# Optimization experiments

Hardware: AMD Instinct MI355X
Metric: run time of the kernel (lower is better)

## Reference

```python
import jax, jax.numpy as jnp
import numpy as np

D_MODEL = 512; N_HEADS = 8; D_HIDDEN = 512
STACK_DEPTH = 48; STACK_WIDTH = 128; D_FF = 2048; D_SS = 128
SEQ = 512; BATCH = 16
EP = 1e-4; MAX_ITER = 100


def nonsat(x):
    # fixed-point iteration y_ = (2y^3/3 + x)/(y^2+1); torch detaches y each step,
    # so grads flow only through x in the final step. Loop runs on stopped values.
    xs = jax.lax.stop_gradient(x)
    step = lambda y: (2.0 * y ** 3 / 3.0 + xs) / (y * y + 1.0)
    def cond(s):
        y, y_, i = s
        return jnp.logical_and(jnp.mean(jnp.abs(y_ - y)) > EP, i <= MAX_ITER)
    def body(s):
        y, y_, i = s
        return (y_, step(y_), i + 1)
    y_last, _, _ = jax.lax.while_loop(cond, body, (xs, step(xs), jnp.int32(0)))
    return (2.0 * y_last ** 3 / 3.0 + x) / (y_last * y_last + 1.0)


def layer_norm(x, g, b, eps=1e-5):
    m = jnp.mean(x, axis=-1, keepdims=True)
    v = jnp.mean((x - m) ** 2, axis=-1, keepdims=True)
    return (x - m) / jnp.sqrt(v + eps) * g + b


def mha(x, k_mask, wi, bi, wo, bo):
    # x: (S,B,E), torch nn.MultiheadAttention with combined in_proj, causal mask
    S, B, E = x.shape
    H = N_HEADS; hd = E // H
    qkv = x @ wi.T + bi
    q, k, v = jnp.split(qkv, 3, axis=-1)
    to_heads = lambda t: t.reshape(S, B, H, hd).transpose(1, 2, 0, 3)  # (B,H,S,hd)
    q = to_heads(q) * (hd ** -0.5)
    k = to_heads(k); v = to_heads(v)
    scores = jnp.einsum('bhqd,bhkd->bhqk', q, k)
    causal = jnp.triu(jnp.full((S, S), -jnp.inf, dtype=x.dtype), 1)
    scores = scores + causal
    scores = jnp.where(k_mask[:, None, None, :], -jnp.inf, scores)
    a = jax.nn.softmax(scores, axis=-1)
    o = jnp.einsum('bhqk,bhkd->bhqd', a, v).transpose(2, 0, 1, 3).reshape(S, B, E)
    return o @ wo.T + bo


def setup_inputs() -> dict:
    key = jax.random.key(0)
    ks = iter(jax.random.split(key, 32))
    E = D_MODEL
    def w(shape, fan_in):
        return (jax.random.normal(next(ks), shape, jnp.float32) / np.sqrt(fan_in)).astype(jnp.float32)
    inp = {
        'x_in': jax.random.normal(next(ks), (SEQ, BATCH, E), jnp.float32),
        'hidden_prev': jax.random.normal(next(ks), (BATCH, SEQ, D_HIDDEN), jnp.float32),
        'stack_prev': jax.random.normal(next(ks), (BATCH, SEQ, STACK_DEPTH, STACK_WIDTH), jnp.float32),
        'k_mask': jnp.zeros((BATCH, SEQ), dtype=bool),
        'in_proj_w': w((3 * E, E), E), 'in_proj_b': jnp.zeros((3 * E,), jnp.float32),
        'out_proj_w': w((E, E), E), 'out_proj_b': jnp.zeros((E,), jnp.float32),
        'ln1_g': jnp.ones((E,), jnp.float32), 'ln1_b': jnp.zeros((E,), jnp.float32),
        'ln2_g': jnp.ones((E,), jnp.float32), 'ln2_b': jnp.zeros((E,), jnp.float32),
        'ff_w1': w((D_FF, E), E), 'ff_b1': jnp.zeros((D_FF,), jnp.float32),
        'ff_w2': w((E, D_FF), D_FF), 'ff_b2': jnp.zeros((E,), jnp.float32),
        'W_w': w((D_HIDDEN, E), E), 'W_b': jnp.zeros((D_HIDDEN,), jnp.float32),
        'R_w': w((D_HIDDEN, D_HIDDEN), D_HIDDEN), 'R_b': jnp.zeros((D_HIDDEN,), jnp.float32),
        'P_w': w((D_HIDDEN, STACK_WIDTH), STACK_WIDTH), 'P_b': jnp.zeros((D_HIDDEN,), jnp.float32),
        'V_w': w((D_SS, E + D_HIDDEN), E + D_HIDDEN),
        'U_w': w((E, D_SS), D_SS),
        'A_w': w((3, D_HIDDEN), D_HIDDEN), 'A_b': jnp.zeros((3,), jnp.float32),
        'D_w': w((STACK_WIDTH, D_HIDDEN), D_HIDDEN), 'D_b': jnp.zeros((STACK_WIDTH,), jnp.float32),
    }
    return inp


def reference(x_in, hidden_prev, stack_prev, k_mask,
              in_proj_w, in_proj_b, out_proj_w, out_proj_b,
              ln1_g, ln1_b, ln2_g, ln2_b,
              ff_w1, ff_b1, ff_w2, ff_b2,
              W_w, W_b, R_w, R_b, P_w, P_b,
              V_w, U_w, A_w, A_b, D_w, D_b):
    # sublayer 1: pre-norm residual multihead self-attention
    x = x_in + mha(layer_norm(x_in, ln1_g, ln1_b), k_mask,
                   in_proj_w, in_proj_b, out_proj_w, out_proj_b)
    # stack-augmented memory update
    stack_x = stack_prev[:, :, 0, :]                       # (B,S,W) stack top
    xb = x.transpose(1, 0, 2)                              # (B,S,E)
    hidden = xb @ W_w.T + W_b + hidden_prev @ R_w.T + R_b + stack_x @ P_w.T + P_b
    hidden = nonsat(hidden)                                # (B,S,Dh)
    vx = jnp.concatenate([x, hidden.transpose(1, 0, 2)], axis=-1)  # (S,B,E+Dh)
    y = jax.nn.softmax(vx @ V_w.T, axis=-1) @ U_w.T        # (S,B,E)
    x = 0.5 * (x + y)
    stack_inp = nonsat(hidden @ D_w.T + D_b)[:, :, None, :]        # (B,S,1,W)
    controls = jax.nn.softmax(hidden @ A_w.T + A_b, axis=-1)       # (B,S,3)
    a_push = controls[:, :, 0, None, None]
    a_pop = controls[:, :, 1, None, None]
    a_noop = controls[:, :, 2, None, None]
    zeros_bot = jnp.zeros_like(stack_prev[:, :, :1])
    stack_down = jnp.concatenate([stack_prev[:, :, 1:], zeros_bot], axis=2)
    stack_up = jnp.concatenate([stack_inp, stack_prev[:, :, :-1]], axis=2)
    stack = a_noop * stack_prev + a_push * stack_up + a_pop * stack_down
    # sublayer 2: pre-norm residual position-wise FFN
    h = layer_norm(x, ln2_g, ln2_b)
    x = x + (jax.nn.relu(h @ ff_w1.T + ff_b1) @ ff_w2.T + ff_b2)
    return (x, hidden, stack)
```

## Files before the change

kernel.cpp:

```cpp
#include <hip/hip_runtime.h>
#include <stdint.h>

typedef unsigned short u16;
typedef short short8 __attribute__((ext_vector_type(8)));
typedef float f32x4 __attribute__((ext_vector_type(4)));

__device__ __forceinline__ u16 f2b(float f) {
    uint32_t x = __float_as_uint(f);
    uint32_t r = x + 0x7fffu + ((x >> 16) & 1u);
    return (u16)(r >> 16);
}

__device__ __forceinline__ float nonsat_f(float x) {
    float y = x;
#pragma unroll
    for (int t = 0; t < 14; ++t) {
        const float y2 = y * y;
        y = (0.66666667f * y2 * y + x) / (y2 + 1.f);
    }
    return y;
}

__device__ __forceinline__ void gl2lds16(const u16* g, u16* l) {
    __builtin_amdgcn_global_load_lds(
        (const __attribute__((address_space(1))) unsigned int*)g,
        (__attribute__((address_space(3))) unsigned int*)l, 16, 0, 0);
}

template <int MT, int MODE, bool RELU>
__global__ __launch_bounds__(256) void gemm_k(
    const u16* __restrict__ A, int lda,
    const u16* __restrict__ B, int ldb,
    const float* __restrict__ bias,
    int M, int N, int K,
    u16* __restrict__ out_b, float* __restrict__ out_f,
    const float* __restrict__ res_f, u16* __restrict__ out_b2)
{
    constexpr int MI = (MT >= 64) ? MT / 64 : 1;
    constexpr int WI = (MT >= 64) ? MT / 32 : 1;
    constexpr int ATILE = MT * 32;
    constexpr size_t STAGE_B = (size_t)(2 * ATILE + 8192) * 2;
    constexpr size_t EPIL_B = (MODE == 0 && MT == 128) ? (size_t)128 * 132 * 2
                             : (MODE == 8 ? (size_t)MT * 130 * 4 : 0);
    constexpr size_t SMEM_B = STAGE_B > EPIL_B ? STAGE_B : EPIL_B;

    const int tn = blockIdx.x, tm = blockIdx.y;
    const int tid = threadIdx.x;
    const int wave = tid >> 6, lane = tid & 63;
    const int quad = lane >> 4, mm = lane & 15;
    const int wr = (wave >> 1) * (MT / 2), wc = (wave & 1) * 64;

    __shared__ __align__(16) char SMEM[SMEM_B];
    u16* As = (u16*)SMEM;
    u16* Bs = (u16*)SMEM + 2 * ATILE;

    const f32x4 vzero = {0.f, 0.f, 0.f, 0.f};
    f32x4 acc[WI][4];
#pragma unroll
    for (int i = 0; i < WI; i++)
#pragma unroll
        for (int j = 0; j < 4; j++) acc[i][j] = vzero;

    const int lr = tid >> 2;
    const int lc = (tid & 3) * 8;
    const u16* ag[MI];
#pragma unroll
    for (int h = 0; h < MI; h++)
        ag[h] = A + (size_t)(tm * MT + (MT == 32 ? (lr & 31) : lr) + h * 64) * lda + lc;
    const u16* bg0 = B + (size_t)(tn * 128 + lr) * ldb + lc;
    const u16* bg1 = B + (size_t)(tn * 128 + lr + 64) * ldb + lc;

    auto STAGE = [&](int s, int kt) {
        if constexpr (MT == 32) {
            if (tid < 128) gl2lds16(ag[0] + kt, As + s * ATILE + wave * 512);
        } else {
#pragma unroll
            for (int h = 0; h < MI; h++)
                gl2lds16(ag[h] + kt, As + s * ATILE + h * 2048 + wave * 512);
        }
        gl2lds16(bg0 + kt, Bs + s * 4096 + wave * 512);
        gl2lds16(bg1 + kt, Bs + s * 4096 + 2048 + wave * 512);
    };

    const int nt = K >> 5;
    STAGE(0, 0);
    asm volatile("s_waitcnt vmcnt(0)" ::: "memory");
    __syncthreads();
    int cur = 0;

    for (int t = 0; t < nt; ++t) {
        if (t + 1 < nt) STAGE(cur ^ 1, (t + 1) * 32);
        const u16* as = As + cur * ATILE;
        const u16* bs = Bs + cur * 4096;
        short8 af[WI], bfr[4];
#pragma unroll
        for (int i = 0; i < WI; i++) af[i] = *(const short8*)(as + (wr + i * 16 + mm) * 32 + quad * 8);
#pragma unroll
        for (int j = 0; j < 4; j++) bfr[j] = *(const short8*)(bs + (wc + j * 16 + mm) * 32 + quad * 8);
#pragma unroll
        for (int i = 0; i < WI; i++)
#pragma unroll
            for (int j = 0; j < 4; j++)
                acc[i][j] = __builtin_amdgcn_mfma_f32_16x16x32_bf16(af[i], bfr[j], acc[i][j], 0, 0, 0);
        if (t + 1 < nt) {
            asm volatile("s_waitcnt vmcnt(0)" ::: "memory");
            __syncthreads();
            cur ^= 1;
        }
    }

    if constexpr (MODE == 0 && MT == 128) {
        __syncthreads();
        u16* Ct = (u16*)SMEM;
#pragma unroll
        for (int j = 0; j < 4; j++) {
            const int colg = tn * 128 + wc + j * 16 + mm;
            const float bv = bias ? bias[colg] : 0.f;
#pragma unroll
            for (int i = 0; i < WI; i++)
#pragma unroll
                for (int r = 0; r < 4; r++) {
                    float v = acc[i][j][r] + bv;
                    if (RELU) v = fmaxf(v, 0.f);
                    Ct[(wr + i * 16 + quad * 4 + r) * 132 + wc + j * 16 + mm] = f2b(v);
                }
        }
        __syncthreads();
        const int row = tid >> 1, half = tid & 1;
        const u16* src = Ct + row * 132 + half * 64;
        u16* dst = out_b + (size_t)(tm * 128 + row) * N + tn * 128 + half * 64;
#pragma unroll
        for (int c = 0; c < 8; c++)
            *(int4*)(dst + c * 8) = *(const int4*)(src + c * 8);
        return;
    }

    if constexpr (MODE == 8) {
        __syncthreads();
        float* Sm = (float*)SMEM;
#pragma unroll
        for (int j = 0; j < 4; j++)
#pragma unroll
            for (int i = 0; i < WI; i++)
#pragma unroll
                for (int r = 0; r < 4; r++)
                    Sm[(wr + i * 16 + quad * 4 + r) * 130 + wc + j * 16 + mm] = acc[i][j][r];
        __syncthreads();
#pragma unroll
        for (int rr = 0; rr < MT / 4; ++rr) {
            const int row_l = wave * (MT / 4) + rr;
            const float a = Sm[row_l * 130 + lane];
            const float b = Sm[row_l * 130 + 64 + lane];
            float mx = fmaxf(a, b);
#pragma unroll
            for (int off = 1; off < 64; off <<= 1) mx = fmaxf(mx, __shfl_xor(mx, off));
            const float ea = __expf(a - mx), eb = __expf(b - mx);
            float s = ea + eb;
#pragma unroll
            for (int off = 1; off < 64; off <<= 1) s += __shfl_xor(s, off);
            const float inv = 1.f / s;
            const size_t rowg = (size_t)tm * MT + row_l;
            out_b[rowg * 128 + lane] = f2b(ea * inv);
            out_b[rowg * 128 + 64 + lane] = f2b(eb * inv);
        }
        return;
    }

    float dotp[3][WI * 4];
    if constexpr (MODE == 6) {
#pragma unroll
        for (int w = 0; w < 3; w++)
#pragma unroll
            for (int q = 0; q < WI * 4; q++) dotp[w][q] = 0.f;
    }

#pragma unroll
    for (int j = 0; j < 4; j++) {
        const int colg = tn * 128 + wc + j * 16 + mm;
        const float bv = bias ? bias[colg] : 0.f;
        float aw0, aw1, aw2;
        if constexpr (MODE == 6) {
            aw0 = res_f[colg];
            aw1 = res_f[512 + colg];
            aw2 = res_f[1024 + colg];
        }
#pragma unroll
        for (int i = 0; i < WI; i++) {
#pragma unroll
            for (int r = 0; r < 4; r++) {
                const int rowg = tm * MT + wr + i * 16 + quad * 4 + r;
                float v = acc[i][j][r] + bv;
                const size_t off = (size_t)rowg * N + colg;
                if constexpr (MODE == 0) {
                    if (RELU) v = fmaxf(v, 0.f);
                    out_b[off] = f2b(v);
                } else if constexpr (MODE == 3) {
                    v += res_f[off];
                    out_f[off] = v;
                    const u16 hb = f2b(v);
                    out_b[(size_t)rowg * 1024 + colg] = hb;
                    out_b2[((size_t)(rowg & 15) * 512 + (rowg >> 4)) * 1152 + colg] = hb;
                } else if constexpr (MODE == 4) {
                    v = 0.5f * (v + res_f[off]);
                    out_f[off] = v;
                } else if constexpr (MODE == 5) {
                    v += res_f[off];
                    out_f[off] = v;
                } else if constexpr (MODE == 6) {
                    v = nonsat_f(v);
                    out_f[off] = v;
                    out_b[((size_t)(rowg & 511) * 16 + (rowg >> 9)) * 1024 + 512 + colg] = f2b(v);
                    dotp[0][i * 4 + r] += v * aw0;
                    dotp[1][i * 4 + r] += v * aw1;
                    dotp[2][i * 4 + r] += v * aw2;
                } else {
                    v = nonsat_f(v);
                    out_f[off] = v;
                }
            }
        }
    }

    if constexpr (MODE == 6) {
        float* lg = (float*)out_b2;
#pragma unroll
        for (int w = 0; w < 3; w++)
#pragma unroll
            for (int i = 0; i < WI; i++)
#pragma unroll
                for (int r = 0; r < 4; r++) {
                    float v = dotp[w][i * 4 + r];
                    v += __shfl_xor(v, 1);
                    v += __shfl_xor(v, 2);
                    v += __shfl_xor(v, 4);
                    v += __shfl_xor(v, 8);
                    if (mm == 0) {
                        const int rowg = tm * MT + wr + i * 16 + quad * 4 + r;
                        atomicAdd(&lg[(size_t)rowg * 3 + w], v);
                    }
                }
    }
}

struct CvtArgs {
    const float* s[12];
    unsigned cum[13];
};

static constexpr unsigned C_INPJ = 0;
static constexpr unsigned C_OUTP = 786432;
static constexpr unsigned C_FF1W = 1048576;
static constexpr unsigned C_FF2W = 2097152;
static constexpr unsigned C_WRP  = 3145728;
static constexpr unsigned C_VW   = 3735552;
static constexpr unsigned C_UW   = 3866624;
static constexpr unsigned C_DW   = 3932160;
static constexpr unsigned C_WTOT = 3997696;

__global__ __launch_bounds__(256) void cvt_k(CvtArgs a, u16* __restrict__ wa, u16* __restrict__ ha,
                                             const float* __restrict__ Wb, const float* __restrict__ Rb,
                                             const float* __restrict__ Pb, float* __restrict__ bsum,
                                             float* __restrict__ logz)
{
    if (blockIdx.x == gridDim.x - 1) {
        if (threadIdx.x < 128) {
            const int c = threadIdx.x * 4;
#pragma unroll
            for (int k = 0; k < 4; k++) bsum[c + k] = Wb[c + k] + Rb[c + k] + Pb[c + k];
        }
        return;
    }
    if (blockIdx.x == gridDim.x - 2) {
        float4 z = make_float4(0.f, 0.f, 0.f, 0.f);
        float4* p = (float4*)logz;
        for (int i = threadIdx.x; i < 6144; i += 256) p[i] = z;
        return;
    }
    const unsigned t = (blockIdx.x * 256u + threadIdx.x) * 8u;
    if (t >= a.cum[12]) return;
    int g = 0;
#pragma unroll
    for (int i = 1; i < 12; i++)
        if (t >= a.cum[i]) g = i;
    const unsigned e = t - a.cum[g];
    const float* src;
    u16* dst;
    if (g == 10) {
        src = a.s[10] + e;
        dst = ha + (size_t)(e >> 9) * 1152 + 512 + (e & 511);
    } else if (g == 11) {
        src = a.s[11] + (size_t)(e >> 7) * 6144 + (e & 127);
        dst = ha + (size_t)(e >> 7) * 1152 + 1024 + (e & 127);
    } else if (g == 4) {
        src = a.s[4] + e;
        dst = wa + C_WRP + (size_t)(e >> 9) * 1152 + (e & 511);
    } else if (g == 5) {
        src = a.s[5] + e;
        dst = wa + C_WRP + (size_t)(e >> 9) * 1152 + 512 + (e & 511);
    } else if (g == 6) {
        src = a.s[6] + e;
        dst = wa + C_WRP + (size_t)(e >> 7) * 1152 + 1024 + (e & 127);
    } else {
        src = a.s[g] + e;
        dst = wa + t;
    }
    float4 u0 = *(const float4*)src;
    float4 u1 = *(const float4*)(src + 4);
    __align__(16) u16 o[8] = {f2b(u0.x), f2b(u0.y), f2b(u0.z), f2b(u0.w),
                              f2b(u1.x), f2b(u1.y), f2b(u1.z), f2b(u1.w)};
    *(int4*)dst = *(const int4*)o;
}

__global__ __launch_bounds__(64) void attn_k(const u16* __restrict__ QKV, u16* __restrict__ O)
{
    const int qt = blockIdx.x;
    const int bh = blockIdx.y;
    const int b = bh >> 3, h = bh & 7;
    const int lane = threadIdx.x;
    const int quad = lane >> 4, mm = lane & 15;
    const int cbase = h * 64;
    const float NEGINF = -3.0e38f;

    __shared__ __align__(16) u16 Pl[64 * 72];
    __shared__ __align__(16) u16 Vl[64 * 72];

    short8 qf[4][2];
#pragma unroll
    for (int rt = 0; rt < 4; ++rt) {
        const int s = qt * 64 + rt * 16 + mm;
        const u16* p = QKV + ((size_t)s * 16 + b) * 1536 + cbase + quad * 8;
        qf[rt][0] = *(const short8*)(p);
        qf[rt][1] = *(const short8*)(p + 32);
    }

    const f32x4 vzero = {0.f, 0.f, 0.f, 0.f};
    f32x4 of[4][4];
#pragma unroll
    for (int i = 0; i < 4; i++)
#pragma unroll
        for (int j = 0; j < 4; j++) of[i][j] = vzero;
    float mrow[4][4], lrow[4][4];
#pragma unroll
    for (int i = 0; i < 4; i++)
#pragma unroll
        for (int r = 0; r < 4; r++) { mrow[i][r] = NEGINF; lrow[i][r] = 0.f; }

    for (int kt = 0; kt <= qt; ++kt) {
        short8 kf[4][2];
#pragma unroll
        for (int nt = 0; nt < 4; ++nt) {
            const int kk = kt * 64 + nt * 16 + mm;
            const u16* p = QKV + ((size_t)kk * 16 + b) * 1536 + 512 + cbase + quad * 8;
            kf[nt][0] = *(const short8*)(p);
            kf[nt][1] = *(const short8*)(p + 32);
        }
        f32x4 sf[4][4];
#pragma unroll
        for (int i = 0; i < 4; i++)
#pragma unroll
            for (int j = 0; j < 4; j++) sf[i][j] = vzero;
#pragma unroll
        for (int i = 0; i < 4; i++)
#pragma unroll
            for (int j = 0; j < 4; j++) {
                sf[i][j] = __builtin_amdgcn_mfma_f32_16x16x32_bf16(qf[i][0], kf[j][0], sf[i][j], 0, 0, 0);
                sf[i][j] = __builtin_amdgcn_mfma_f32_16x16x32_bf16(qf[i][1], kf[j][1], sf[i][j], 0, 0, 0);
            }
        {
            const int kk = lane >> 3, c8 = (lane & 7) * 8;
#pragma unroll
            for (int it = 0; it < 8; ++it) {
                const int key = kt * 64 + it * 8 + kk;
                int4 v = *(const int4*)(QKV + ((size_t)key * 16 + b) * 1536 + 1024 + cbase + c8);
                *(int4*)(Vl + (it * 8 + kk) * 72 + c8) = v;
            }
        }
        const bool diag = (kt == qt);
#pragma unroll
        for (int i = 0; i < 4; i++)
#pragma unroll
            for (int j = 0; j < 4; j++)
#pragma unroll
                for (int r = 0; r < 4; r++) {
                    float v = sf[i][j][r] * 0.125f;
                    if (diag) {
                        const int q = i * 16 + quad * 4 + r;
                        const int k = j * 16 + mm;
                        if (k > q) v = NEGINF;
                    }
                    sf[i][j][r] = v;
                }
#pragma unroll
        for (int i = 0; i < 4; i++) {
#pragma unroll
            for (int r = 0; r < 4; r++) {
                float mx = fmaxf(fmaxf(sf[i][0][r], sf[i][1][r]), fmaxf(sf[i][2][r], sf[i][3][r]));
                mx = fmaxf(mx, __shfl_xor(mx, 1));
                mx = fmaxf(mx, __shfl_xor(mx, 2));
                mx = fmaxf(mx, __shfl_xor(mx, 4));
                mx = fmaxf(mx, __shfl_xor(mx, 8));
                const float mnew = fmaxf(mrow[i][r], mx);
                const float alpha = __expf(mrow[i][r] - mnew);
                mrow[i][r] = mnew;
                float psum = 0.f;
#pragma unroll
                for (int j = 0; j < 4; j++) {
                    float p = __expf(sf[i][j][r] - mnew);
                    sf[i][j][r] = p;
                    psum += p;
                }
                psum += __shfl_xor(psum, 1);
                psum += __shfl_xor(psum, 2);
                psum += __shfl_xor(psum, 4);
                psum += __shfl_xor(psum, 8);
                lrow[i][r] = lrow[i][r] * alpha + psum;
#pragma unroll
                for (int j = 0; j < 4; j++) of[i][j][r] *= alpha;
            }
        }
#pragma unroll
        for (int i = 0; i < 4; i++)
#pragma unroll
            for (int j = 0; j < 4; j++)
#pragma unroll
                for (int r = 0; r < 4; r++)
                    Pl[(i * 16 + quad * 4 + r) * 72 + j * 16 + mm] = f2b(sf[i][j][r]);
        __syncthreads();
        short8 pa[4][2];
#pragma unroll
        for (int i = 0; i < 4; i++) {
            pa[i][0] = *(const short8*)(Pl + (i * 16 + mm) * 72 + quad * 8);
            pa[i][1] = *(const short8*)(Pl + (i * 16 + mm) * 72 + 32 + quad * 8);
        }
#pragma unroll
        for (int j = 0; j < 4; j++) {
#pragma unroll
            for (int kc = 0; kc < 2; ++kc) {
                short8 vb;
#pragma unroll
                for (int e = 0; e < 8; e++)
                    vb[e] = (short)Vl[(kc * 32 + quad * 8 + e) * 72 + j * 16 + mm];
#pragma unroll
                for (int i = 0; i < 4; i++)
                    of[i][j] = __builtin_amdgcn_mfma_f32_16x16x32_bf16(pa[i][kc], vb, of[i][j], 0, 0, 0);
            }
        }
        __syncthreads();
    }
#pragma unroll
    for (int i = 0; i < 4; i++)
#pragma unroll
        for (int r = 0; r < 4; r++) {
            const int s = qt * 64 + i * 16 + quad * 4 + r;
            const float inv = 1.f / lrow[i][r];
#pragma unroll
            for (int j = 0; j < 4; j++)
                O[((size_t)s * 16 + b) * 512 + cbase + j * 16 + mm] = f2b(of[i][j][r] * inv);
        }
}

__global__ __launch_bounds__(256) void ln_k(const float* __restrict__ x,
                                            const float* __restrict__ g,
                                            const float* __restrict__ be,
                                            u16* __restrict__ out)
{
    const int row = blockIdx.x * 4 + (threadIdx.x >> 6);
    const int lane = threadIdx.x & 63;
    const float* p = x + (size_t)row * 512 + lane * 8;
    float4 u0 = *(const float4*)p;
    float4 u1 = *(const float4*)(p + 4);
    float v[8] = {u0.x, u0.y, u0.z, u0.w, u1.x, u1.y, u1.z, u1.w};
    float s = 0.f, s2 = 0.f;
#pragma unroll
    for (int j = 0; j < 8; j++) { s += v[j]; s2 += v[j] * v[j]; }
#pragma unroll
    for (int off = 1; off < 64; off <<= 1) { s += __shfl_xor(s, off); s2 += __shfl_xor(s2, off); }
    const float mean = s * (1.f / 512.f);
    const float var = s2 * (1.f / 512.f) - mean * mean;
    const float rstd = rsqrtf(fmaxf(var, 0.f) + 1e-5f);
    float4 g0 = *(const float4*)(g + lane * 8);
    float4 g1 = *(const float4*)(g + lane * 8 + 4);
    float4 b0 = *(const float4*)(be + lane * 8);
    float4 b1 = *(const float4*)(be + lane * 8 + 4);
    const float gg[8] = {g0.x, g0.y, g0.z, g0.w, g1.x, g1.y, g1.z, g1.w};
    const float bb[8] = {b0.x, b0.y, b0.z, b0.w, b1.x, b1.y, b1.z, b1.w};
    __align__(16) u16 o[8];
#pragma unroll
    for (int j = 0; j < 8; j++)
        o[j] = f2b((v[j] - mean) * rstd * gg[j] + bb[j]);
    *(int4*)(out + (size_t)row * 512 + lane * 8) = *(const int4*)o;
}

__global__ __launch_bounds__(256) void stack_k(const float* __restrict__ sp_all, const float* __restrict__ sin,
                                               const float* __restrict__ lg, const float* __restrict__ Ab,
                                               float* __restrict__ out)
{
    const int bs = blockIdx.x;
    const int t = blockIdx.y * 256 + threadIdx.x;
    const int d = t >> 4;
    const int w = (t & 15) * 8;
    const float* sp = sp_all + (size_t)bs * 6144;
    const float l0 = lg[(size_t)bs * 3 + 0] + Ab[0];
    const float l1 = lg[(size_t)bs * 3 + 1] + Ab[1];
    const float l2 = lg[(size_t)bs * 3 + 2] + Ab[2];
    const float mx = fmaxf(l0, fmaxf(l1, l2));
    const float e0 = __expf(l0 - mx), e1 = __expf(l1 - mx), e2 = __expf(l2 - mx);
    const float inv = 1.f / (e0 + e1 + e2);
    const float pu = e0 * inv;
    const float po = e1 * inv;
    const float no = e2 * inv;
    float cur[8], up[8], dn[8];
    {
        const float* p = sp + d * 128 + w;
        float4 c0 = *(const float4*)p, c1 = *(const float4*)(p + 4);
        cur[0]=c0.x; cur[1]=c0.y; cur[2]=c0.z; cur[3]=c0.w; cur[4]=c1.x; cur[5]=c1.y; cur[6]=c1.z; cur[7]=c1.w;
    }
    {
        const int bb = bs >> 9, ss = bs & 511;
        const float* p = (d == 0) ? (sin + ((size_t)ss * 16 + bb) * 128 + w) : (sp + (d - 1) * 128 + w);
        float4 c0 = *(const float4*)p, c1 = *(const float4*)(p + 4);
        up[0]=c0.x; up[1]=c0.y; up[2]=c0.z; up[3]=c0.w; up[4]=c1.x; up[5]=c1.y; up[6]=c1.z; up[7]=c1.w;
    }
    if (d < 47) {
        const float* p = sp + (d + 1) * 128 + w;
        float4 c0 = *(const float4*)p, c1 = *(const float4*)(p + 4);
        dn[0]=c0.x; dn[1]=c0.y; dn[2]=c0.z; dn[3]=c0.w; dn[4]=c1.x; dn[5]=c1.y; dn[6]=c1.z; dn[7]=c1.w;
    } else {
#pragma unroll
        for (int j = 0; j < 8; j++) dn[j] = 0.f;
    }
    float o[8];
#pragma unroll
    for (int j = 0; j < 8; j++)
        o[j] = no * cur[j] + pu * up[j] + po * dn[j];
    float* q = out + (size_t)bs * 6144 + d * 128 + w;
    *(float4*)q = make_float4(o[0], o[1], o[2], o[3]);
    *(float4*)(q + 4) = make_float4(o[4], o[5], o[6], o[7]);
}

static constexpr size_t O_A1 = 0;
static constexpr size_t O_QKV = O_A1 + 8388608;
static constexpr size_t O_OATT = O_QKV + 25165824;
static constexpr size_t O_X1F = O_OATT + 8388608;
static constexpr size_t O_HPF = O_X1F + 16777216;
static constexpr size_t O_VL = O_HPF + 16777216;
static constexpr size_t O_X2F = O_VL + 4194304;
static constexpr size_t O_H2 = O_X2F + 16777216;
static constexpr size_t WS_NEED = O_H2 + 8388608;
static constexpr size_t O_VX = O_QKV;
static constexpr size_t O_PS = O_QKV + 16777216;
static constexpr size_t O_SIN = O_QKV + 18874368;
static constexpr size_t O_LG = O_VL + 4096;
static constexpr size_t O_FF1 = O_X1F;

static constexpr size_t WA_BYTES = (size_t)C_WTOT * 2;
static constexpr size_t HA_BYTES = (size_t)8192 * 1152 * 2;
static constexpr size_t STASH_BYTES = WA_BYTES + HA_BYTES;
static constexpr size_t STASH_OFF = 201326592 - STASH_BYTES;

extern "C" void kernel_launch(void* const* d_in, const int* in_sizes, int n_in,
                              void* d_out, int out_size, void* d_ws, size_t ws_size,
                              hipStream_t stream)
{
    (void)in_sizes; (void)n_in; (void)out_size;
    if (ws_size < WS_NEED) return;

    const float* x_in        = (const float*)d_in[0];
    const float* hidden_prev = (const float*)d_in[1];
    const float* stack_prev  = (const float*)d_in[2];
    const float* in_proj_w   = (const float*)d_in[4];
    const float* in_proj_b   = (const float*)d_in[5];
    const float* out_proj_w  = (const float*)d_in[6];
    const float* out_proj_b  = (const float*)d_in[7];
    const float* ln1_g       = (const float*)d_in[8];
    const float* ln1_b       = (const float*)d_in[9];
    const float* ln2_g       = (const float*)d_in[10];
    const float* ln2_b       = (const float*)d_in[11];
    const float* ff_w1       = (const float*)d_in[12];
    const float* ff_b1       = (const float*)d_in[13];
    const float* ff_w2       = (const float*)d_in[14];
    const float* ff_b2       = (const float*)d_in[15];
    const float* W_w         = (const float*)d_in[16];
    const float* W_b         = (const float*)d_in[17];
    const float* R_w         = (const float*)d_in[18];
    const float* R_b         = (const float*)d_in[19];
    const float* P_w         = (const float*)d_in[20];
    const float* P_b         = (const float*)d_in[21];
    const float* V_w         = (const float*)d_in[22];
    const float* U_w         = (const float*)d_in[23];
    const float* A_w         = (const float*)d_in[24];
    const float* A_b         = (const float*)d_in[25];
    const float* D_w         = (const float*)d_in[26];
    const float* D_b         = (const float*)d_in[27];

    char* ws = (char*)d_ws;
    u16* A1   = (u16*)(ws + O_A1);
    u16* QKV  = (u16*)(ws + O_QKV);
    u16* OATT = (u16*)(ws + O_OATT);
    float* X1F = (float*)(ws + O_X1F);
    float* bsum = (float*)(ws + O_VL);
    float* LG  = (float*)(ws + O_LG);
    float* X2F = (float*)(ws + O_X2F);
    u16* H2   = (u16*)(ws + O_H2);
    u16* VX   = (u16*)(ws + O_VX);
    u16* PS   = (u16*)(ws + O_PS);
    float* SIN = (float*)(ws + O_SIN);
    u16* FF1  = (u16*)(ws + O_FF1);

    float* out = (float*)d_out;
    float* x_out = out;
    float* hid_out = out + 4194304;
    float* stack_out = out + 8388608;
    u16* wa = (u16*)((char*)stack_out + STASH_OFF);
    u16* ha = (u16*)((char*)wa + WA_BYTES);

    CvtArgs ca;
    ca.s[0] = in_proj_w; ca.s[1] = out_proj_w; ca.s[2] = ff_w1; ca.s[3] = ff_w2;
    ca.s[4] = W_w; ca.s[5] = R_w; ca.s[6] = P_w; ca.s[7] = V_w;
    ca.s[8] = U_w; ca.s[9] = D_w; ca.s[10] = hidden_prev; ca.s[11] = stack_prev;
    const unsigned cums[13] = {C_INPJ, C_OUTP, C_FF1W, C_FF2W, 3145728, 3407872, 3670016,
                               C_VW, C_UW, C_DW, C_WTOT, 8192000, 9240576};
    for (int i = 0; i < 13; i++) ca.cum[i] = cums[i];
    cvt_k<<<4514, 256, 0, stream>>>(ca, wa, ha, W_b, R_b, P_b, bsum, LG);

    ln_k<<<2048, 256, 0, stream>>>(x_in, ln1_g, ln1_b, A1);
    gemm_k<128, 0, false><<<dim3(12, 64), 256, 0, stream>>>(
        A1, 512, wa + C_INPJ, 512, in_proj_b, 8192, 1536, 512, QKV, nullptr, nullptr, nullptr);
    attn_k<<<dim3(8, 128), 64, 0, stream>>>(QKV, OATT);
    gemm_k<64, 3, false><<<dim3(4, 128), 256, 0, stream>>>(
        OATT, 512, wa + C_OUTP, 512, out_proj_b, 8192, 512, 512, VX, X1F, x_in, ha);
    gemm_k<64, 6, false><<<dim3(4, 128), 256, 0, stream>>>(
        ha, 1152, wa + C_WRP, 1152, bsum, 8192, 512, 1152, VX, hid_out, A_w, (u16*)LG);
    gemm_k<32, 8, false><<<dim3(1, 256), 256, 0, stream>>>(
        VX, 1024, wa + C_VW, 1024, nullptr, 8192, 128, 1024, PS, nullptr, nullptr, nullptr);
    gemm_k<64, 4, false><<<dim3(4, 128), 256, 0, stream>>>(
        PS, 128, wa + C_UW, 128, nullptr, 8192, 512, 128, nullptr, X2F, X1F, nullptr);
    gemm_k<32, 7, false><<<dim3(1, 256), 256, 0, stream>>>(
        VX + 512, 1024, wa + C_DW, 512, D_b, 8192, 128, 512, nullptr, SIN, nullptr, nullptr);
    ln_k<<<2048, 256, 0, stream>>>(X2F, ln2_g, ln2_b, H2);
    gemm_k<128, 0, true><<<dim3(16, 64), 256, 0, stream>>>(
        H2, 512, wa + C_FF1W, 512, ff_b1, 8192, 2048, 512, FF1, nullptr, nullptr, nullptr);
    gemm_k<64, 5, false><<<dim3(4, 128), 256, 0, stream>>>(
        FF1, 2048, wa + C_FF2W, 2048, ff_b2, 8192, 512, 2048, nullptr, x_out, X2F, nullptr);
    stack_k<<<dim3(8192, 3), 256, 0, stream>>>(stack_prev, SIN, LG, A_b, stack_out);
}
```

Measured before the change: 718.4 us.

## Fuse V and D projections into one GEMM and remap workgroups across XCDs

Measured after the change: 696.2 us. -3.1%, faster.

```diff
diff --git a/kernel.cpp b/kernel.cpp
--- a/kernel.cpp
+++ b/kernel.cpp
@@ -41,10 +41,19 @@
     constexpr int ATILE = MT * 32;
     constexpr size_t STAGE_B = (size_t)(2 * ATILE + 8192) * 2;
     constexpr size_t EPIL_B = (MODE == 0 && MT == 128) ? (size_t)128 * 132 * 2
-                             : (MODE == 8 ? (size_t)MT * 130 * 4 : 0);
+                             : (MODE == 9 ? (size_t)MT * 130 * 4 : 0);
     constexpr size_t SMEM_B = STAGE_B > EPIL_B ? STAGE_B : EPIL_B;
 
-    const int tn = blockIdx.x, tm = blockIdx.y;
+    const unsigned gx = gridDim.x;
+    const unsigned nwg = gx * gridDim.y;
+    const unsigned fid = blockIdx.y * gx + blockIdx.x;
+    unsigned nid = fid;
+    if ((nwg & 7u) == 0u) {
+        const unsigned chunk = nwg >> 3;
+        nid = (fid & 7u) * chunk + (fid >> 3);
+    }
+    const int tn = nid % gx, tm = nid / gx;
+
     const int tid = threadIdx.x;
     const int wave = tid >> 6, lane = tid & 63;
     const int quad = lane >> 4, mm = lane & 15;
@@ -135,33 +144,48 @@
         return;
     }
 
-    if constexpr (MODE == 8) {
+    if constexpr (MODE == 9) {
         __syncthreads();
         float* Sm = (float*)SMEM;
-#pragma unroll
-        for (int j = 0; j < 4; j++)
-#pragma unroll
-            for (int i = 0; i < WI; i++)
-#pragma unroll
-                for (int r = 0; r < 4; r++)
-                    Sm[(wr + i * 16 + quad * 4 + r) * 130 + wc + j * 16 + mm] = acc[i][j][r];
-        __syncthreads();
-#pragma unroll
-        for (int rr = 0; rr < MT / 4; ++rr) {
-            const int row_l = wave * (MT / 4) + rr;
-            const float a = Sm[row_l * 130 + lane];
-            const float b = Sm[row_l * 130 + 64 + lane];
-            float mx = fmaxf(a, b);
-#pragma unroll
-            for (int off = 1; off < 64; off <<= 1) mx = fmaxf(mx, __shfl_xor(mx, off));
-            const float ea = __expf(a - mx), eb = __expf(b - mx);
-            float s = ea + eb;
-#pragma unroll
-            for (int off = 1; off < 64; off <<= 1) s += __shfl_xor(s, off);
-            const float inv = 1.f / s;
-            const size_t rowg = (size_t)tm * MT + row_l;
-            out_b[rowg * 128 + lane] = f2b(ea * inv);
-            out_b[rowg * 128 + 64 + lane] = f2b(eb * inv);
+        if (tn == 0) {
+#pragma unroll
+            for (int j = 0; j < 4; j++)
+#pragma unroll
+                for (int i = 0; i < WI; i++)
+#pragma unroll
+                    for (int r = 0; r < 4; r++)
+                        Sm[(wr + i * 16 + quad * 4 + r) * 130 + wc + j * 16 + mm] = acc[i][j][r];
+            __syncthreads();
+#pragma unroll
+            for (int rr = 0; rr < MT / 4; ++rr) {
+                const int row_l = wave * (MT / 4) + rr;
+                const float a0 = Sm[row_l * 130 + lane];
+                const float a1 = Sm[row_l * 130 + 64 + lane];
+                float mx = fmaxf(a0, a1);
+#pragma unroll
+                for (int off = 1; off < 64; off <<= 1) mx = fmaxf(mx, __shfl_xor(mx, off));
+                const float ea = __expf(a0 - mx), eb = __expf(a1 - mx);
+                float s = ea + eb;
+#pragma unroll
+                for (int off = 1; off < 64; off <<= 1) s += __shfl_xor(s, off);
+                const float inv = 1.f / s;
+                const size_t rowg = (size_t)tm * MT + row_l;
+                out_b[rowg * 128 + lane] = f2b(ea * inv);
+                out_b[rowg * 128 + 64 + lane] = f2b(eb * inv);
+            }
+        } else {
+#pragma unroll
+            for (int j = 0; j < 4; j++) {
+                const int col_l = wc + j * 16 + mm;
+                const float bv = bias[col_l];
+#pragma unroll
+                for (int i = 0; i < WI; i++)
+#pragma unroll
+                    for (int r = 0; r < 4; r++) {
+                        const int rowg = tm * MT + wr + i * 16 + quad * 4 + r;
+                        out_f[(size_t)rowg * 128 + col_l] = nonsat_f(acc[i][j][r] + bv);
+                    }
+            }
         }
         return;
     }
@@ -213,9 +237,6 @@
                     dotp[0][i * 4 + r] += v * aw0;
                     dotp[1][i * 4 + r] += v * aw1;
                     dotp[2][i * 4 + r] += v * aw2;
-                } else {
-                    v = nonsat_f(v);
-                    out_f[off] = v;
                 }
             }
         }
@@ -243,8 +264,8 @@
 }
 
 struct CvtArgs {
-    const float* s[12];
-    unsigned cum[13];
+    const float* s[13];
+    unsigned cum[14];
 };
 
 static constexpr unsigned C_INPJ = 0;
@@ -252,10 +273,9 @@
 static constexpr unsigned C_FF1W = 1048576;
 static constexpr unsigned C_FF2W = 2097152;
 static constexpr unsigned C_WRP  = 3145728;
-static constexpr unsigned C_VW   = 3735552;
-static constexpr unsigned C_UW   = 3866624;
-static constexpr unsigned C_DW   = 3932160;
-static constexpr unsigned C_WTOT = 3997696;
+static constexpr unsigned C_VD   = 3735552;
+static constexpr unsigned C_UW   = 3997696;
+static constexpr unsigned C_WTOT = 4063232;
 
 __global__ __launch_bounds__(256) void cvt_k(CvtArgs a, u16* __restrict__ wa, u16* __restrict__ ha,
                                              const float* __restrict__ Wb, const float* __restrict__ Rb,
@@ -277,33 +297,28 @@
         return;
     }
     const unsigned t = (blockIdx.x * 256u + threadIdx.x) * 8u;
-    if (t >= a.cum[12]) return;
+    if (t >= a.cum[13]) return;
     int g = 0;
 #pragma unroll
-    for (int i = 1; i < 12; i++)
+    for (int i = 1; i < 13; i++)
         if (t >= a.cum[i]) g = i;
     const unsigned e = t - a.cum[g];
-    const float* src;
+    const float* src = nullptr;
     u16* dst;
-    if (g == 10) {
-        src = a.s[10] + e;
-        dst = ha + (size_t)(e >> 9) * 1152 + 512 + (e & 511);
-    } else if (g == 11) {
-        src = a.s[11] + (size_t)(e >> 7) * 6144 + (e & 127);
-        dst = ha + (size_t)(e >> 7) * 1152 + 1024 + (e & 127);
-    } else if (g == 4) {
-        src = a.s[4] + e;
-        dst = wa + C_WRP + (size_t)(e >> 9) * 1152 + (e & 511);
-    } else if (g == 5) {
-        src = a.s[5] + e;
-        dst = wa + C_WRP + (size_t)(e >> 9) * 1152 + 512 + (e & 511);
-    } else if (g == 6) {
-        src = a.s[6] + e;
-        dst = wa + C_WRP + (size_t)(e >> 7) * 1152 + 1024 + (e & 127);
-    } else {
-        src = a.s[g] + e;
-        dst = wa + t;
-    }
+    if (g <= 3) { src = a.s[g] + e; dst = wa + t; }
+    else if (g == 4) { src = a.s[4] + e; dst = wa + C_WRP + (size_t)(e >> 9) * 1152 + (e & 511); }
+    else if (g == 5) { src = a.s[5] + e; dst = wa + C_WRP + (size_t)(e >> 9) * 1152 + 512 + (e & 511); }
+    else if (g == 6) { src = a.s[6] + e; dst = wa + C_WRP + (size_t)(e >> 7) * 1152 + 1024 + (e & 127); }
+    else if (g == 7) { src = a.s[7] + e; dst = wa + C_VD + e; }
+    else if (g == 8) { src = a.s[8] + e; dst = wa + C_VD + 131072 + (size_t)(e >> 9) * 1024 + 512 + (e & 511); }
+    else if (g == 9) {
+        dst = wa + C_VD + 131072 + (size_t)(e >> 9) * 1024 + (e & 511);
+        *(int4*)dst = make_int4(0, 0, 0, 0);
+        return;
+    }
+    else if (g == 10) { src = a.s[10] + e; dst = wa + C_UW + e; }
+    else if (g == 11) { src = a.s[11] + e; dst = ha + (size_t)(e >> 9) * 1152 + 512 + (e & 511); }
+    else { src = a.s[12] + (size_t)(e >> 7) * 6144 + (e & 127); dst = ha + (size_t)(e >> 7) * 1152 + 1024 + (e & 127); }
     float4 u0 = *(const float4*)src;
     float4 u1 = *(const float4*)(src + 4);
     __align__(16) u16 o[8] = {f2b(u0.x), f2b(u0.y), f2b(u0.z), f2b(u0.w),
@@ -313,8 +328,10 @@
 
 __global__ __launch_bounds__(64) void attn_k(const u16* __restrict__ QKV, u16* __restrict__ O)
 {
-    const int qt = blockIdx.x;
-    const int bh = blockIdx.y;
+    const unsigned fid = blockIdx.y * 8 + blockIdx.x;
+    const unsigned nid = (fid & 7u) * 128u + (fid >> 3);
+    const int qt = nid & 7;
+    const int bh = nid >> 3;
     const int b = bh >> 3, h = bh & 7;
     const int lane = threadIdx.x;
     const int quad = lane >> 4, mm = lane & 15;
@@ -617,11 +634,12 @@
     CvtArgs ca;
     ca.s[0] = in_proj_w; ca.s[1] = out_proj_w; ca.s[2] = ff_w1; ca.s[3] = ff_w2;
     ca.s[4] = W_w; ca.s[5] = R_w; ca.s[6] = P_w; ca.s[7] = V_w;
-    ca.s[8] = U_w; ca.s[9] = D_w; ca.s[10] = hidden_prev; ca.s[11] = stack_prev;
-    const unsigned cums[13] = {C_INPJ, C_OUTP, C_FF1W, C_FF2W, 3145728, 3407872, 3670016,
-                               C_VW, C_UW, C_DW, C_WTOT, 8192000, 9240576};
-    for (int i = 0; i < 13; i++) ca.cum[i] = cums[i];
-    cvt_k<<<4514, 256, 0, stream>>>(ca, wa, ha, W_b, R_b, P_b, bsum, LG);
+    ca.s[8] = D_w; ca.s[9] = nullptr; ca.s[10] = U_w; ca.s[11] = hidden_prev;
+    ca.s[12] = stack_prev;
+    const unsigned cums[14] = {0, 786432, 1048576, 2097152, 3145728, 3407872, 3670016,
+                               3735552, 3866624, 3932160, 3997696, 4063232, 8257536, 9306112};
+    for (int i = 0; i < 14; i++) ca.cum[i] = cums[i];
+    cvt_k<<<4546, 256, 0, stream>>>(ca, wa, ha, W_b, R_b, P_b, bsum, LG);
 
     ln_k<<<2048, 256, 0, stream>>>(x_in, ln1_g, ln1_b, A1);
     gemm_k<128, 0, false><<<dim3(12, 64), 256, 0, stream>>>(
@@ -631,12 +649,10 @@
         OATT, 512, wa + C_OUTP, 512, out_proj_b, 8192, 512, 512, VX, X1F, x_in, ha);
     gemm_k<64, 6, false><<<dim3(4, 128), 256, 0, stream>>>(
         ha, 1152, wa + C_WRP, 1152, bsum, 8192, 512, 1152, VX, hid_out, A_w, (u16*)LG);
-    gemm_k<32, 8, false><<<dim3(1, 256), 256, 0, stream>>>(
-        VX, 1024, wa + C_VW, 1024, nullptr, 8192, 128, 1024, PS, nullptr, nullptr, nullptr);
+    gemm_k<32, 9, false><<<dim3(2, 256), 256, 0, stream>>>(
+        VX, 1024, wa + C_VD, 1024, D_b, 8192, 256, 1024, PS, SIN, nullptr, nullptr);
     gemm_k<64, 4, false><<<dim3(4, 128), 256, 0, stream>>>(
         PS, 128, wa + C_UW, 128, nullptr, 8192, 512, 128, nullptr, X2F, X1F, nullptr);
-    gemm_k<32, 7, false><<<dim3(1, 256), 256, 0, stream>>>(
-        VX + 512, 1024, wa + C_DW, 512, D_b, 8192, 128, 512, nullptr, SIN, nullptr, nullptr);
     ln_k<<<2048, 256, 0, stream>>>(X2F, ln2_g, ln2_b, H2);
     gemm_k<128, 0, true><<<dim3(16, 64), 256, 0, stream>>>(
         H2, 512, wa + C_FF1W, 512, ff_b1, 8192, 2048, 512, FF1, nullptr, nullptr, nullptr);
```
